# Optimization experiments

Measured on AMD Instinct MI355X. Metric: run time of the kernel, lower is better.

## Reference

```python
import math
import jax, jax.numpy as jnp
import numpy as np

B, N, D, H = 2, 8192, 1024, 16


def setup_inputs() -> dict:
    key = jax.random.key(0)
    k1, k2, k3, k4 = jax.random.split(key, 4)
    s = 1.0 / math.sqrt(D)
    return {
        "x": jax.random.normal(k1, (B, N, D), dtype=jnp.float32),
        "W_qk": jax.random.normal(k2, (D, D), dtype=jnp.float32) * s,
        "W_v": jax.random.normal(k3, (D, D), dtype=jnp.float32) * s,
        "W_out": jax.random.normal(k4, (D, D), dtype=jnp.float32) * s,
        "tau": jnp.ones((H, 1, 1), dtype=jnp.float32),
    }


def reference(x, W_qk, W_v, W_out, tau):
    b, n, d = x.shape
    h = H
    dh = d // h
    # QK / V projections (no bias), then to channel-major (B, H, dh, N)
    qk = (x @ W_qk).transpose(0, 2, 1).reshape(b, h, dh, n)
    v = (x @ W_v).transpose(0, 2, 1).reshape(b, h, dh, n)
    # Cross-channel Gram matrix over tokens: (B, H, dh, dh)
    dot = jnp.einsum('bhcn,bhdn->bhcd', qk, qk)
    q2 = jnp.sum(qk * qk, axis=-1)  # (B, H, dh)
    # Negative squared Euclidean distance between channel vectors
    logits = (2.0 * dot - q2[:, :, :, None] - q2[:, :, None, :]) / math.sqrt(max(n, 1))
    logits = logits * tau[None, ...]
    attn = jax.nn.softmax(logits, axis=-1)  # (B, H, dh, dh)
    w = jnp.einsum('bhcd,bhdn->bhcn', attn, v)  # (B, H, dh, N)
    out = w.reshape(b, d, n).transpose(0, 2, 1) @ W_out  # (B, N, D)
    return out
```

## Files before the change

### kernel.cpp

```cpp
#include <hip/hip_runtime.h>
#include <hip/hip_bf16.h>
#include <cstdint>
#include <cstddef>

typedef __bf16 v8bf __attribute__((ext_vector_type(8)));
typedef float  v4f  __attribute__((ext_vector_type(4)));

__device__ __forceinline__ unsigned short f2bf(float f) {
    unsigned int u = __float_as_uint(f);
    u += 0x7fffu + ((u >> 16) & 1u);
    return (unsigned short)(u >> 16);
}

__device__ __forceinline__ void gload_lds16(const unsigned short* g, unsigned short* l) {
    __builtin_amdgcn_global_load_lds(
        (const __attribute__((address_space(1))) unsigned int*)(uintptr_t)g,
        (__attribute__((address_space(3))) unsigned int*)(uintptr_t)l, 16, 0, 0);
}

template<int WRITE_BF16>
__global__ __launch_bounds__(256, 2) void gemm_bt(
    const unsigned short* __restrict__ A,
    const unsigned short* __restrict__ BT,
    void* __restrict__ C,
    int K, int lda, int ldb, int ldc,
    size_t sAz, size_t sBz, size_t sCz)
{
    __shared__ unsigned short sA[128 * 32];
    __shared__ unsigned short sB[128 * 32];

    const unsigned short* Ab = A + (size_t)blockIdx.z * sAz;
    const unsigned short* Bb = BT + (size_t)blockIdx.z * sBz;

    const int tid  = threadIdx.x;
    const int wv   = tid >> 6;
    const int lane = tid & 63;
    const int quad = lane >> 4;
    const int l16  = lane & 15;
    const size_t bm = (size_t)blockIdx.y * 128;
    const size_t bn = (size_t)blockIdx.x * 128;
    const int wm = (wv >> 1) * 64;
    const int wn = (wv & 1) * 64;

    const int ro = tid >> 2;
    const int ko = (tid & 3) << 3;

    const unsigned short* aptr0 = Ab + (bm + ro)      * (size_t)lda + ko;
    const unsigned short* aptr1 = Ab + (bm + ro + 64) * (size_t)lda + ko;
    const unsigned short* bptr0 = Bb + (bn + ro)      * (size_t)ldb + ko;
    const unsigned short* bptr1 = Bb + (bn + ro + 64) * (size_t)ldb + ko;

    unsigned short* sA0 = &sA[wv * 512];
    unsigned short* sA1 = &sA[2048 + wv * 512];
    unsigned short* sB0 = &sB[wv * 512];
    unsigned short* sB1 = &sB[2048 + wv * 512];

    v4f acc[4][4] = {};

    for (int k0 = 0; k0 < K; k0 += 32) {
        gload_lds16(aptr0 + k0, sA0);
        gload_lds16(aptr1 + k0, sA1);
        gload_lds16(bptr0 + k0, sB0);
        gload_lds16(bptr1 + k0, sB1);
        __syncthreads();

        v8bf af[4], bfr[4];
        #pragma unroll
        for (int t = 0; t < 4; t++) {
            af[t]  = *(const v8bf*)&sA[(size_t)(wm + t * 16 + l16) * 32 + quad * 8];
            bfr[t] = *(const v8bf*)&sB[(size_t)(wn + t * 16 + l16) * 32 + quad * 8];
        }

        #pragma unroll
        for (int ti = 0; ti < 4; ti++)
            #pragma unroll
            for (int tj = 0; tj < 4; tj++)
                acc[ti][tj] = __builtin_amdgcn_mfma_f32_16x16x32_bf16(
                    af[ti], bfr[tj], acc[ti][tj], 0, 0, 0);
        __syncthreads();
    }

    if (WRITE_BF16) {
        unsigned short* Cb = (unsigned short*)C + (size_t)blockIdx.z * sCz;
        #pragma unroll
        for (int ti = 0; ti < 4; ti++) {
            const size_t row0 = bm + wm + ti * 16 + quad * 4;
            #pragma unroll
            for (int tj = 0; tj < 4; tj++) {
                const size_t col = bn + wn + tj * 16 + l16;
                #pragma unroll
                for (int r = 0; r < 4; r++)
                    Cb[(row0 + r) * (size_t)ldc + col] = f2bf(acc[ti][tj][r]);
            }
        }
    } else {
        float* Cb = (float*)C + (size_t)blockIdx.z * sCz;
        #pragma unroll
        for (int ti = 0; ti < 4; ti++) {
            const size_t row0 = bm + wm + ti * 16 + quad * 4;
            #pragma unroll
            for (int tj = 0; tj < 4; tj++) {
                const size_t col = bn + wn + tj * 16 + l16;
                #pragma unroll
                for (int r = 0; r < 4; r++)
                    Cb[(row0 + r) * (size_t)ldc + col] = acc[ti][tj][r];
            }
        }
    }
}

__global__ __launch_bounds__(256) void gram_kernel(
    const unsigned short* __restrict__ qkv,
    float* __restrict__ partial)
{
    const int bh = blockIdx.x;
    const int split = blockIdx.y;
    const int b = bh >> 4, h = bh & 15;
    const unsigned short* base = qkv + (size_t)b * 8192 * 2048 + (size_t)h * 64;
    const int n0 = split * 1024;

    __shared__ unsigned short sMT[64 * 136];
    const int tid = threadIdx.x;
    const int wv = tid >> 6, lane = tid & 63, quad = lane >> 4, l16 = lane & 15;

    v4f acc[4] = {};

    for (int chunk = 0; chunk < 8; chunk++) {
        const int nb = n0 + chunk * 128;
        __syncthreads();
        #pragma unroll
        for (int i = 0; i < 4; i++) {
            const int ch = tid + i * 256;
            const int tok = ch >> 3;
            const int co = (ch & 7) << 3;
            union { uint4 v; unsigned short s[8]; } u;
            u.v = *(const uint4*)(base + (size_t)(nb + tok) * 2048 + co);
            #pragma unroll
            for (int j = 0; j < 8; j++)
                sMT[(size_t)(co + j) * 136 + tok] = u.s[j];
        }
        __syncthreads();

        #pragma unroll
        for (int ks = 0; ks < 4; ks++) {
            const int kb = ks * 32 + quad * 8;
            const v8bf a = *(const v8bf*)&sMT[(size_t)(16 * wv + l16) * 136 + kb];
            #pragma unroll
            for (int t = 0; t < 4; t++) {
                const v8bf bb = *(const v8bf*)&sMT[(size_t)(t * 16 + l16) * 136 + kb];
                acc[t] = __builtin_amdgcn_mfma_f32_16x16x32_bf16(a, bb, acc[t], 0, 0, 0);
            }
        }
    }

    float* outp = partial + ((size_t)split * 32 + bh) * 4096;
    #pragma unroll
    for (int t = 0; t < 4; t++)
        #pragma unroll
        for (int r = 0; r < 4; r++)
            outp[(size_t)(16 * wv + quad * 4 + r) * 64 + t * 16 + l16] = acc[t][r];
}

__global__ __launch_bounds__(256) void softmax_kernel(
    const float* __restrict__ partial,
    const float* __restrict__ tau,
    float* __restrict__ attn)
{
    const int gw = (int)((blockIdx.x * 256 + threadIdx.x) >> 6);
    const int d = threadIdx.x & 63;
    const int bh = gw >> 6;
    const int c = gw & 63;
    const int h = bh & 15;

    float cd = 0.f, cc = 0.f, dd = 0.f;
    #pragma unroll
    for (int s = 0; s < 8; s++) {
        const float* p = partial + ((size_t)s * 32 + bh) * 4096;
        cd += p[c * 64 + d];
        cc += p[c * 65];
        dd += p[d * 65];
    }
    const float INV_SQRT_N = 0.011048543456039806f;
    const float logit = (2.f * cd - cc - dd) * INV_SQRT_N * tau[h];

    float m = logit;
    #pragma unroll
    for (int off = 32; off > 0; off >>= 1) m = fmaxf(m, __shfl_xor(m, off, 64));
    const float e = __expf(logit - m);
    float sum = e;
    #pragma unroll
    for (int off = 32; off > 0; off >>= 1) sum += __shfl_xor(sum, off, 64);

    attn[(size_t)bh * 4096 + c * 64 + d] = e / sum;
}

__global__ __launch_bounds__(256) void wefft_kernel(
    const float* __restrict__ attn,
    const float* __restrict__ Wout,
    unsigned short* __restrict__ weffT)
{
    const int bh = blockIdx.x;
    const int jg = blockIdx.y;
    const int b = bh >> 4, h = bh & 15;

    __shared__ float sAttT[64][65];
    __shared__ float sW[64][65];
    const int tid = threadIdx.x;
    const float* ap = attn + (size_t)bh * 4096;
    const float* wp = Wout + (size_t)(h * 64) * 1024 + jg * 64;
    for (int i = tid; i < 4096; i += 256) {
        const int cc = i >> 6, q = i & 63;
        sAttT[q][cc] = ap[i];
        sW[cc][q] = wp[(size_t)cc * 1024 + q];
    }
    __syncthreads();

    const int dd0 = (tid >> 4) << 2;
    const int j0  = (tid & 15) << 2;
    float acc[4][4] = {};
    for (int cc = 0; cc < 64; cc++) {
        float av[4], wvv[4];
        #pragma unroll
        for (int i = 0; i < 4; i++) av[i] = sAttT[dd0 + i][cc];
        #pragma unroll
        for (int i = 0; i < 4; i++) wvv[i] = sW[cc][j0 + i];
        #pragma unroll
        for (int i = 0; i < 4; i++)
            #pragma unroll
            for (int j = 0; j < 4; j++)
                acc[i][j] += av[i] * wvv[j];
    }

    unsigned short* op = weffT + ((size_t)b * 1024 + jg * 64) * 1024 + h * 64;
    #pragma unroll
    for (int i = 0; i < 4; i++)
        #pragma unroll
        for (int j = 0; j < 4; j++)
            op[(size_t)(j0 + j) * 1024 + dd0 + i] = f2bf(acc[i][j]);
}

__global__ __launch_bounds__(256) void cvt_x_kernel(
    const float* __restrict__ x, unsigned short* __restrict__ xb)
{
    const size_t i = ((size_t)blockIdx.x * 256 + threadIdx.x) * 4;
    const float4 v = *(const float4*)(x + i);
    ushort4 o;
    o.x = f2bf(v.x); o.y = f2bf(v.y); o.z = f2bf(v.z); o.w = f2bf(v.w);
    *(ushort4*)(xb + i) = o;
}

__global__ void cvt_wT_kernel(const float* __restrict__ W0,
                              const float* __restrict__ W1,
                              unsigned short* __restrict__ WT)
{
    const float* W = blockIdx.z ? W1 : W0;
    unsigned short* O = WT + (size_t)blockIdx.z * 1024 * 1024;
    __shared__ float s[32][33];
    const int n0 = blockIdx.x * 32;
    const int k0 = blockIdx.y * 32;
    for (int i = threadIdx.y; i < 32; i += 8)
        s[i][threadIdx.x] = W[(size_t)(k0 + i) * 1024 + n0 + threadIdx.x];
    __syncthreads();
    for (int i = threadIdx.y; i < 32; i += 8)
        O[(size_t)(n0 + i) * 1024 + k0 + threadIdx.x] = f2bf(s[threadIdx.x][i]);
}

extern "C" void kernel_launch(void* const* d_in, const int* in_sizes, int n_in,
                              void* d_out, int out_size, void* d_ws, size_t ws_size,
                              hipStream_t stream)
{
    (void)in_sizes; (void)n_in; (void)out_size; (void)ws_size;
    const float* x    = (const float*)d_in[0];
    const float* Wqk  = (const float*)d_in[1];
    const float* Wv   = (const float*)d_in[2];
    const float* Wout = (const float*)d_in[3];
    const float* tau  = (const float*)d_in[4];

    unsigned short* xb  = (unsigned short*)d_ws;
    unsigned short* wT  = xb + (size_t)16384 * 1024;
    unsigned short* qkv = wT + (size_t)2048 * 1024;
    unsigned short* wefT = xb;
    float* partial = (float*)(xb + (size_t)2 * 1024 * 1024);
    float* attn    = partial + (size_t)8 * 32 * 4096;

    cvt_x_kernel<<<16384, 256, 0, stream>>>(x, xb);
    cvt_wT_kernel<<<dim3(32, 32, 2), dim3(32, 8), 0, stream>>>(Wqk, Wv, wT);
    gemm_bt<1><<<dim3(16, 128, 1), 256, 0, stream>>>(
        xb, wT, (void*)qkv, 1024, 1024, 1024, 2048, 0, 0, 0);
    gram_kernel<<<dim3(32, 8), 256, 0, stream>>>(qkv, partial);
    softmax_kernel<<<512, 256, 0, stream>>>(partial, tau, attn);
    wefft_kernel<<<dim3(32, 16), 256, 0, stream>>>(attn, Wout, wefT);
    gemm_bt<0><<<dim3(8, 64, 2), 256, 0, stream>>>(
        qkv + 1024, wefT, d_out, 1024, 2048, 1024, 1024,
        (size_t)8192 * 2048, (size_t)1024 * 1024, (size_t)8192 * 1024);
}
```

Measured before the change: 293.4 us.

## Fold W_v into per-batch output weight and swizzle GEMM LDS layout

Instead of projecting x through W_v for all tokens, the code precomputes a per-batch folded weight (W_v times the attention-weighted W_out) with a small GEMM. The final GEMM then multiplies x directly by that weight. This removes half of the large projection GEMM and the V intermediate's memory traffic, at the cost of one small extra GEMM launch. It also adds an XOR swizzle to the GEMM's LDS tile layout to reduce bank conflicts on fragment reads.

Result: faster. 280.9 us (-4.3%).

```diff
diff --git a/kernel.cpp b/kernel.cpp
--- a/kernel.cpp
+++ b/kernel.cpp
@@ -43,7 +43,7 @@
     const int wn = (wv & 1) * 64;
 
     const int ro = tid >> 2;
-    const int ko = (tid & 3) << 3;
+    const int ko = (((tid & 3) ^ (ro & 3)) << 3);
 
     const unsigned short* aptr0 = Ab + (bm + ro)      * (size_t)lda + ko;
     const unsigned short* aptr1 = Ab + (bm + ro + 64) * (size_t)lda + ko;
@@ -54,6 +54,8 @@
     unsigned short* sA1 = &sA[2048 + wv * 512];
     unsigned short* sB0 = &sB[wv * 512];
     unsigned short* sB1 = &sB[2048 + wv * 512];
+
+    const int sslot = ((quad ^ (l16 & 3)) << 3);
 
     v4f acc[4][4] = {};
 
@@ -67,8 +69,8 @@
         v8bf af[4], bfr[4];
         #pragma unroll
         for (int t = 0; t < 4; t++) {
-            af[t]  = *(const v8bf*)&sA[(size_t)(wm + t * 16 + l16) * 32 + quad * 8];
-            bfr[t] = *(const v8bf*)&sB[(size_t)(wn + t * 16 + l16) * 32 + quad * 8];
+            af[t]  = *(const v8bf*)&sA[(size_t)(wm + t * 16 + l16) * 32 + sslot];
+            bfr[t] = *(const v8bf*)&sB[(size_t)(wn + t * 16 + l16) * 32 + sslot];
         }
 
         #pragma unroll
@@ -110,13 +112,13 @@
 }
 
 __global__ __launch_bounds__(256) void gram_kernel(
-    const unsigned short* __restrict__ qkv,
+    const unsigned short* __restrict__ qk,
     float* __restrict__ partial)
 {
     const int bh = blockIdx.x;
     const int split = blockIdx.y;
     const int b = bh >> 4, h = bh & 15;
-    const unsigned short* base = qkv + (size_t)b * 8192 * 2048 + (size_t)h * 64;
+    const unsigned short* base = qk + (size_t)b * 8192 * 1024 + (size_t)h * 64;
     const int n0 = split * 1024;
 
     __shared__ unsigned short sMT[64 * 136];
@@ -134,7 +136,7 @@
             const int tok = ch >> 3;
             const int co = (ch & 7) << 3;
             union { uint4 v; unsigned short s[8]; } u;
-            u.v = *(const uint4*)(base + (size_t)(nb + tok) * 2048 + co);
+            u.v = *(const uint4*)(base + (size_t)(nb + tok) * 1024 + co);
             #pragma unroll
             for (int j = 0; j < 8; j++)
                 sMT[(size_t)(co + j) * 136 + tok] = u.s[j];
@@ -249,12 +251,9 @@
     *(ushort4*)(xb + i) = o;
 }
 
-__global__ void cvt_wT_kernel(const float* __restrict__ W0,
-                              const float* __restrict__ W1,
+__global__ void cvt_wT_kernel(const float* __restrict__ W,
                               unsigned short* __restrict__ WT)
 {
-    const float* W = blockIdx.z ? W1 : W0;
-    unsigned short* O = WT + (size_t)blockIdx.z * 1024 * 1024;
     __shared__ float s[32][33];
     const int n0 = blockIdx.x * 32;
     const int k0 = blockIdx.y * 32;
@@ -262,7 +261,7 @@
         s[i][threadIdx.x] = W[(size_t)(k0 + i) * 1024 + n0 + threadIdx.x];
     __syncthreads();
     for (int i = threadIdx.y; i < 32; i += 8)
-        O[(size_t)(n0 + i) * 1024 + k0 + threadIdx.x] = f2bf(s[threadIdx.x][i]);
+        WT[(size_t)(n0 + i) * 1024 + k0 + threadIdx.x] = f2bf(s[threadIdx.x][i]);
 }
 
 extern "C" void kernel_launch(void* const* d_in, const int* in_sizes, int n_in,
@@ -276,21 +275,31 @@
     const float* Wout = (const float*)d_in[3];
     const float* tau  = (const float*)d_in[4];
 
-    unsigned short* xb  = (unsigned short*)d_ws;
-    unsigned short* wT  = xb + (size_t)16384 * 1024;
-    unsigned short* qkv = wT + (size_t)2048 * 1024;
-    unsigned short* wefT = xb;
-    float* partial = (float*)(xb + (size_t)2 * 1024 * 1024);
-    float* attn    = partial + (size_t)8 * 32 * 4096;
+    unsigned short* xb     = (unsigned short*)d_ws;
+    unsigned short* wqkT   = xb + (size_t)16384 * 1024;
+    unsigned short* wvb    = wqkT + (size_t)1024 * 1024;
+    unsigned short* qk     = wvb + (size_t)1024 * 1024;
+    float*          partial= (float*)(qk + (size_t)16384 * 1024);
+    float*          attn   = partial + (size_t)8 * 32 * 4096;
+    unsigned short* weffT  = (unsigned short*)(attn + (size_t)32 * 4096);
+    unsigned short* wfoldT = weffT + (size_t)2 * 1024 * 1024;
 
     cvt_x_kernel<<<16384, 256, 0, stream>>>(x, xb);
-    cvt_wT_kernel<<<dim3(32, 32, 2), dim3(32, 8), 0, stream>>>(Wqk, Wv, wT);
-    gemm_bt<1><<<dim3(16, 128, 1), 256, 0, stream>>>(
-        xb, wT, (void*)qkv, 1024, 1024, 1024, 2048, 0, 0, 0);
-    gram_kernel<<<dim3(32, 8), 256, 0, stream>>>(qkv, partial);
+    cvt_x_kernel<<<1024, 256, 0, stream>>>(Wv, wvb);
+    cvt_wT_kernel<<<dim3(32, 32), dim3(32, 8), 0, stream>>>(Wqk, wqkT);
+
+    gemm_bt<1><<<dim3(8, 128, 1), 256, 0, stream>>>(
+        xb, wqkT, (void*)qk, 1024, 1024, 1024, 1024, 0, 0, 0);
+
+    gram_kernel<<<dim3(32, 8), 256, 0, stream>>>(qk, partial);
     softmax_kernel<<<512, 256, 0, stream>>>(partial, tau, attn);
-    wefft_kernel<<<dim3(32, 16), 256, 0, stream>>>(attn, Wout, wefT);
+    wefft_kernel<<<dim3(32, 16), 256, 0, stream>>>(attn, Wout, weffT);
+
+    gemm_bt<1><<<dim3(8, 8, 2), 256, 0, stream>>>(
+        weffT, wvb, (void*)wfoldT, 1024, 1024, 1024, 1024,
+        (size_t)1024 * 1024, 0, (size_t)1024 * 1024);
+
     gemm_bt<0><<<dim3(8, 64, 2), 256, 0, stream>>>(
-        qkv + 1024, wefT, d_out, 1024, 2048, 1024, 1024,
-        (size_t)8192 * 2048, (size_t)1024 * 1024, (size_t)8192 * 1024);
-}
+        xb, wfoldT, d_out, 1024, 1024, 1024, 1024,
+        (size_t)8192 * 1024, (size_t)1024 * 1024, (size_t)8192 * 1024);
+}
```
